# Performance work log

Measured on AMD Instinct MI355X. Metric: run time of the kernel, lower is better.

Reference implementation:

```python
import jax, jax.numpy as jnp
import numpy as np

N_NODES = 100000
N_EDGES = 640000
IN_CH = 128
HID = 128


def setup_inputs() -> dict:
    key = jax.random.key(0)
    k1, k2, k3, k4, k5 = jax.random.split(key, 5)
    z = jax.random.normal(k1, (N_NODES, IN_CH), dtype=jnp.float32)
    edge_index = jax.random.randint(k2, (2, N_EDGES), 0, N_NODES, dtype=jnp.int64)
    # Linear layers: stored as [in, out] for x @ W + b
    s1 = 1.0 / np.sqrt(2 * IN_CH)
    W1 = jax.random.uniform(k3, (2 * IN_CH, HID), minval=-s1, maxval=s1, dtype=jnp.float32)
    b1 = jnp.zeros((HID,), dtype=jnp.float32)
    s2 = 1.0 / np.sqrt(HID)
    W2 = jax.random.uniform(k4, (HID, 1), minval=-s2, maxval=s2, dtype=jnp.float32)
    b2 = jnp.zeros((1,), dtype=jnp.float32)
    return {"z": z, "edge_index": edge_index, "W1": W1, "b1": b1, "W2": W2, "b2": b2}


def reference(z, edge_index, W1, b1, W2, b2):
    # gather source/destination node embeddings and concat -> [E, 2*C]
    h = jnp.concatenate([z[edge_index[0]], z[edge_index[1]]], axis=-1)
    h = jax.nn.relu(h @ W1 + b1)  # [E, HID]; Dropout(0.2) is identity in eval
    out = h @ W2 + b2             # [E, 1]
    return out.squeeze(-1)        # [E]
```

## Files before the change

### kernel.cpp

```cpp
#include <hip/hip_runtime.h>
#include <hip/hip_bf16.h>

typedef short bf16x8 __attribute__((ext_vector_type(8)));
typedef float f32x4  __attribute__((ext_vector_type(4)));
typedef unsigned short u16;

static __device__ __forceinline__ u16 f2bf(float f) {
    unsigned u = __float_as_uint(f);
    u += 0x7FFFu + ((u >> 16) & 1u);
    return (u16)(u >> 16);
}
static __device__ __forceinline__ float bf2f(u16 b) {
    return __uint_as_float(((unsigned)b) << 16);
}
static __device__ __forceinline__ unsigned pack2(float lo, float hi) {
    return (unsigned)f2bf(lo) | ((unsigned)f2bf(hi) << 16);
}

#define BM 64
__global__ __launch_bounds__(256, 2) void node_gemm(
    const float* __restrict__ z,
    const float* __restrict__ W1,
    const float* __restrict__ b1,
    u16*         __restrict__ PQ,
    int M, int ntiles)
{
    __shared__ char As[BM * 256];
    __shared__ char Cb[BM * 512];
    const int tid  = threadIdx.x;
    const int lane = tid & 63;
    const int wave = tid >> 6;
    const int g    = lane >> 4;
    const int ln   = lane & 15;
    const int c0   = wave * 64;

    int t = blockIdx.x;
    if (t >= ntiles) return;

    bf16x8 af[4][4];
    #pragma unroll
    for (int ci = 0; ci < 4; ++ci) {
        int c = c0 + ci * 16 + ln;
        const float* src = (c < 128) ? (W1 + c) : (W1 + 128 * 128 + (c - 128));
        #pragma unroll
        for (int ks = 0; ks < 4; ++ks) {
            bf16x8 v;
            #pragma unroll
            for (int j = 0; j < 8; ++j)
                v[j] = (short)f2bf(src[(ks * 32 + g * 8 + j) * 128]);
            af[ks][ci] = v;
        }
    }

    float4 bias[4];
    #pragma unroll
    for (int ci = 0; ci < 4; ++ci) {
        int col = c0 + ci * 16 + g * 4;
        bias[ci] = (col < 128) ? *(const float4*)(b1 + col)
                               : make_float4(0.f, 0.f, 0.f, 0.f);
    }

    float4 r[8];

    {
        int m0 = t * BM;
        #pragma unroll
        for (int i = 0; i < 8; ++i) {
            int ci = tid + i * 256, row = ci >> 5, c4 = ci & 31;
            r[i] = make_float4(0.f, 0.f, 0.f, 0.f);
            if (m0 + row < M)
                r[i] = *(const float4*)(z + (size_t)(m0 + row) * 128 + c4 * 4);
        }
        #pragma unroll
        for (int i = 0; i < 8; ++i) {
            int ci = tid + i * 256, row = ci >> 5, c4 = ci & 31;
            ushort4 b;
            b.x = f2bf(r[i].x); b.y = f2bf(r[i].y);
            b.z = f2bf(r[i].z); b.w = f2bf(r[i].w);
            *(ushort4*)(As + row * 256 + ((c4 * 8) ^ ((row & 7) << 4))) = b;
        }
    }
    __syncthreads();

    while (true) {
        int next = t + gridDim.x;
        bool have = (next < ntiles);

        if (have) {
            int m0 = next * BM;
            #pragma unroll
            for (int i = 0; i < 8; ++i) {
                int ci = tid + i * 256, row = ci >> 5, c4 = ci & 31;
                r[i] = make_float4(0.f, 0.f, 0.f, 0.f);
                if (m0 + row < M)
                    r[i] = *(const float4*)(z + (size_t)(m0 + row) * 128 + c4 * 4);
            }
        }

        f32x4 acc[4][4];
        #pragma unroll
        for (int mf = 0; mf < 4; ++mf)
            #pragma unroll
            for (int ci = 0; ci < 4; ++ci)
                acc[mf][ci] = (f32x4){0.f, 0.f, 0.f, 0.f};
        #pragma unroll
        for (int ks = 0; ks < 4; ++ks) {
            #pragma unroll
            for (int mf = 0; mf < 4; ++mf) {
                int row  = mf * 16 + ln;
                int byte = row * 256 + ((ks * 64 + g * 16) ^ ((row & 7) << 4));
                bf16x8 b = *(const bf16x8*)(As + byte);
                #pragma unroll
                for (int ci = 0; ci < 4; ++ci)
                    acc[mf][ci] = __builtin_amdgcn_mfma_f32_16x16x32_bf16(
                        af[ks][ci], b, acc[mf][ci], 0, 0, 0);
            }
        }

        #pragma unroll
        for (int mf = 0; mf < 4; ++mf) {
            int node = mf * 16 + ln;
            #pragma unroll
            for (int ci = 0; ci < 4; ++ci) {
                int col = c0 + ci * 16 + g * 4;
                uint2 w;
                w.x = pack2(acc[mf][ci][0] + bias[ci].x,
                            acc[mf][ci][1] + bias[ci].y);
                w.y = pack2(acc[mf][ci][2] + bias[ci].z,
                            acc[mf][ci][3] + bias[ci].w);
                *(uint2*)(Cb + node * 512 + ((col * 2) ^ ((node & 7) << 4))) = w;
            }
        }
        __syncthreads();

        {
            int m0 = t * BM;
            int chunk = tid & 31;
            int nb    = tid >> 5;
            #pragma unroll
            for (int it = 0; it < 8; ++it) {
                int node = it * 8 + nb;
                uint4 v = *(const uint4*)(Cb + node * 512 +
                                          ((chunk * 16) ^ ((node & 7) << 4)));
                if (m0 + node < M)
                    *(uint4*)(PQ + (size_t)(m0 + node) * 256 + chunk * 8) = v;
            }
        }

        if (have) {
            #pragma unroll
            for (int i = 0; i < 8; ++i) {
                int ci = tid + i * 256, row = ci >> 5, c4 = ci & 31;
                ushort4 b;
                b.x = f2bf(r[i].x); b.y = f2bf(r[i].y);
                b.z = f2bf(r[i].z); b.w = f2bf(r[i].w);
                *(ushort4*)(As + row * 256 + ((c4 * 8) ^ ((row & 7) << 4))) = b;
            }
        } else {
            break;
        }
        __syncthreads();
        t = next;
    }
}

__global__ __launch_bounds__(256) void edge_mlp(
    const int* __restrict__ ei,
    const u16* __restrict__ PQ,
    const float* __restrict__ W2,
    const float* __restrict__ b2,
    float* __restrict__ out,
    int E)
{
    int gid = blockIdx.x * 256 + threadIdx.x;
    int e0  = (gid >> 4) * 4;
    int sub = gid & 15;
    if (e0 >= E) return;

    float4 w2a = *(const float4*)(W2 + sub * 8);
    float4 w2b = *(const float4*)(W2 + sub * 8 + 4);
    float ww[8] = {w2a.x, w2a.y, w2a.z, w2a.w, w2b.x, w2b.y, w2b.z, w2b.w};
    float bias = b2[0];

    if (e0 + 3 < E) {
        int4 s = *(const int4*)(ei + e0);
        int4 d = *(const int4*)(ei + E + e0);
        uint4 p0 = *(const uint4*)(PQ + (size_t)s.x * 256 + sub * 8);
        uint4 p1 = *(const uint4*)(PQ + (size_t)s.y * 256 + sub * 8);
        uint4 p2 = *(const uint4*)(PQ + (size_t)s.z * 256 + sub * 8);
        uint4 p3 = *(const uint4*)(PQ + (size_t)s.w * 256 + sub * 8);
        uint4 q0 = *(const uint4*)(PQ + (size_t)d.x * 256 + 128 + sub * 8);
        uint4 q1 = *(const uint4*)(PQ + (size_t)d.y * 256 + 128 + sub * 8);
        uint4 q2 = *(const uint4*)(PQ + (size_t)d.z * 256 + 128 + sub * 8);
        uint4 q3 = *(const uint4*)(PQ + (size_t)d.w * 256 + 128 + sub * 8);

        float a0 = 0.f, a1 = 0.f, a2 = 0.f, a3 = 0.f;
        const u16* pu0 = (const u16*)&p0; const u16* qu0 = (const u16*)&q0;
        const u16* pu1 = (const u16*)&p1; const u16* qu1 = (const u16*)&q1;
        const u16* pu2 = (const u16*)&p2; const u16* qu2 = (const u16*)&q2;
        const u16* pu3 = (const u16*)&p3; const u16* qu3 = (const u16*)&q3;
        #pragma unroll
        for (int j = 0; j < 8; ++j) {
            a0 = fmaf(fmaxf(bf2f(pu0[j]) + bf2f(qu0[j]), 0.f), ww[j], a0);
            a1 = fmaf(fmaxf(bf2f(pu1[j]) + bf2f(qu1[j]), 0.f), ww[j], a1);
            a2 = fmaf(fmaxf(bf2f(pu2[j]) + bf2f(qu2[j]), 0.f), ww[j], a2);
            a3 = fmaf(fmaxf(bf2f(pu3[j]) + bf2f(qu3[j]), 0.f), ww[j], a3);
        }
        #pragma unroll
        for (int m = 1; m < 16; m <<= 1) {
            a0 += __shfl_xor(a0, m);
            a1 += __shfl_xor(a1, m);
            a2 += __shfl_xor(a2, m);
            a3 += __shfl_xor(a3, m);
        }
        if (sub == 0) {
            float4 o = make_float4(a0 + bias, a1 + bias, a2 + bias, a3 + bias);
            *(float4*)(out + e0) = o;
        }
    } else {
        for (int k = 0; k < 4; ++k) {
            int e = e0 + k;
            if (e >= E) break;
            int sn = ei[e], dn = ei[E + e];
            uint4 p = *(const uint4*)(PQ + (size_t)sn * 256 + sub * 8);
            uint4 q = *(const uint4*)(PQ + (size_t)dn * 256 + 128 + sub * 8);
            const u16* pu = (const u16*)&p; const u16* qu = (const u16*)&q;
            float acc = 0.f;
            #pragma unroll
            for (int j = 0; j < 8; ++j)
                acc = fmaf(fmaxf(bf2f(pu[j]) + bf2f(qu[j]), 0.f), ww[j], acc);
            #pragma unroll
            for (int m = 1; m < 16; m <<= 1) acc += __shfl_xor(acc, m);
            if (sub == 0) out[e] = acc + bias;
        }
    }
}

extern "C" void kernel_launch(void* const* d_in, const int* in_sizes, int n_in,
                              void* d_out, int out_size, void* d_ws, size_t ws_size,
                              hipStream_t stream) {
    const float* z  = (const float*)d_in[0];
    const int*   ei = (const int*)d_in[1];
    const float* W1 = (const float*)d_in[2];
    const float* b1 = (const float*)d_in[3];
    const float* W2 = (const float*)d_in[4];
    const float* b2 = (const float*)d_in[5];
    float* out = (float*)d_out;

    const int M = in_sizes[0] / 128;
    const int E = in_sizes[1] / 2;

    u16* PQ = (u16*)d_ws;

    int ntiles = (M + BM - 1) / BM;
    int gb = ntiles < 512 ? ntiles : 512;
    hipLaunchKernelGGL(node_gemm, dim3(gb), dim3(256), 0, stream,
                       z, W1, b1, PQ, M, ntiles);

    int eb = ((E + 3) / 4 * 16 + 255) / 256;
    hipLaunchKernelGGL(edge_mlp, dim3(eb), dim3(256), 0, stream,
                       ei, PQ, W2, b2, out, E);
}
```

Baseline: 71.80 us.

## Partition edges by source-node range per block to localize gathers

Adds an edge kernel in which each of 8 block groups scans edge chunks, compacts via ballot and shared-memory queue the edges whose source node falls in its node range, then gathers P/Q rows and computes outputs. The goal is to improve cache locality of source-row gathers, possibly per XCD. It costs an 8x re-read of source indices, extra syncs and atomics, and scattered output writes. The fallback kernel is simplified to a scalar per-edge loop.

```diff
diff --git a/kernel.cpp b/kernel.cpp
--- a/kernel.cpp
+++ b/kernel.cpp
@@ -4,6 +4,7 @@
 typedef short bf16x8 __attribute__((ext_vector_type(8)));
 typedef float f32x4  __attribute__((ext_vector_type(4)));
 typedef unsigned short u16;
+typedef unsigned long long u64;
 
 static __device__ __forceinline__ u16 f2bf(float f) {
     unsigned u = __float_as_uint(f);
@@ -61,7 +62,6 @@
     }
 
     float4 r[8];
-
     {
         int m0 = t * BM;
         #pragma unroll
@@ -164,75 +164,153 @@
     }
 }
 
-__global__ __launch_bounds__(256) void edge_mlp(
+#define FCH 2048
+__global__ __launch_bounds__(256) void edge_mlp_filter(
     const int* __restrict__ ei,
     const u16* __restrict__ PQ,
     const float* __restrict__ W2,
     const float* __restrict__ b2,
     float* __restrict__ out,
-    int E)
+    int E, int M)
+{
+    __shared__ u64 q[512];
+    __shared__ int qn;
+    __shared__ int pn;
+
+    const int tid  = threadIdx.x;
+    const int myb  = blockIdx.x & 7;
+    const int chnk = blockIdx.x >> 3;
+    const int bsz  = (M + 7) >> 3;
+    const int lo   = myb * bsz;
+    const int hi   = (lo + bsz < M) ? (lo + bsz) : M;
+    const int sub  = tid & 15;
+    const int grp  = tid >> 4;
+
+    float4 w2a = *(const float4*)(W2 + sub * 8);
+    float4 w2b = *(const float4*)(W2 + sub * 8 + 4);
+    float ww[8] = {w2a.x, w2a.y, w2a.z, w2a.w, w2b.x, w2b.y, w2b.z, w2b.w};
+    float bias = b2[0];
+
+    if (tid == 0) qn = 0;
+    __syncthreads();
+
+    const int e0 = chnk * FCH;
+    #pragma unroll 1
+    for (int r = 0; r < FCH / 256; ++r) {
+        int e = e0 + r * 256 + tid;
+        int s = 0, d = 0;
+        bool mine = false;
+        if (e < E) {
+            s = ei[e];
+            if (s >= lo && s < hi) { mine = true; d = ei[E + e]; }
+        }
+        u64 mask = __ballot(mine);
+        int rank = __popcll(mask & ((1ULL << (tid & 63)) - 1ULL));
+        int wcnt = __popcll(mask);
+        int wb = 0;
+        if ((tid & 63) == 0 && wcnt) wb = atomicAdd(&qn, wcnt);
+        wb = __shfl(wb, 0);
+        if (mine)
+            q[wb + rank] = (u64)(unsigned)s | ((u64)(unsigned)d << 17)
+                         | ((u64)(unsigned)e << 34);
+        __syncthreads();
+
+        bool flush = (qn > 256) || (r == FCH / 256 - 1);
+        if (flush) {
+            if (tid == 0) { pn = qn; qn = 0; }
+            __syncthreads();
+            int n = pn;
+            for (int base = grp * 4; base < n; base += 64) {
+                if (base + 4 <= n) {
+                    u64 v0 = q[base], v1 = q[base + 1];
+                    u64 v2 = q[base + 2], v3 = q[base + 3];
+                    unsigned s0 = (unsigned)(v0 & 0x1FFFF), d0 = (unsigned)((v0 >> 17) & 0x1FFFF);
+                    unsigned s1 = (unsigned)(v1 & 0x1FFFF), d1 = (unsigned)((v1 >> 17) & 0x1FFFF);
+                    unsigned s2 = (unsigned)(v2 & 0x1FFFF), d2 = (unsigned)((v2 >> 17) & 0x1FFFF);
+                    unsigned s3 = (unsigned)(v3 & 0x1FFFF), d3 = (unsigned)((v3 >> 17) & 0x1FFFF);
+                    uint4 p0 = *(const uint4*)(PQ + (size_t)s0 * 256 + sub * 8);
+                    uint4 p1 = *(const uint4*)(PQ + (size_t)s1 * 256 + sub * 8);
+                    uint4 p2 = *(const uint4*)(PQ + (size_t)s2 * 256 + sub * 8);
+                    uint4 p3 = *(const uint4*)(PQ + (size_t)s3 * 256 + sub * 8);
+                    uint4 q0 = *(const uint4*)(PQ + (size_t)d0 * 256 + 128 + sub * 8);
+                    uint4 q1 = *(const uint4*)(PQ + (size_t)d1 * 256 + 128 + sub * 8);
+                    uint4 q2 = *(const uint4*)(PQ + (size_t)d2 * 256 + 128 + sub * 8);
+                    uint4 q3 = *(const uint4*)(PQ + (size_t)d3 * 256 + 128 + sub * 8);
+                    float a0 = 0.f, a1 = 0.f, a2 = 0.f, a3 = 0.f;
+                    const u16* pu0 = (const u16*)&p0; const u16* qu0 = (const u16*)&q0;
+                    const u16* pu1 = (const u16*)&p1; const u16* qu1 = (const u16*)&q1;
+                    const u16* pu2 = (const u16*)&p2; const u16* qu2 = (const u16*)&q2;
+                    const u16* pu3 = (const u16*)&p3; const u16* qu3 = (const u16*)&q3;
+                    #pragma unroll
+                    for (int j = 0; j < 8; ++j) {
+                        a0 = fmaf(fmaxf(bf2f(pu0[j]) + bf2f(qu0[j]), 0.f), ww[j], a0);
+                        a1 = fmaf(fmaxf(bf2f(pu1[j]) + bf2f(qu1[j]), 0.f), ww[j], a1);
+                        a2 = fmaf(fmaxf(bf2f(pu2[j]) + bf2f(qu2[j]), 0.f), ww[j], a2);
+                        a3 = fmaf(fmaxf(bf2f(pu3[j]) + bf2f(qu3[j]), 0.f), ww[j], a3);
+                    }
+                    #pragma unroll
+                    for (int m = 1; m < 16; m <<= 1) {
+                        a0 += __shfl_xor(a0, m);
+                        a1 += __shfl_xor(a1, m);
+                        a2 += __shfl_xor(a2, m);
+                        a3 += __shfl_xor(a3, m);
+                    }
+                    if (sub == 0) {
+                        out[(unsigned)(v0 >> 34)] = a0 + bias;
+                        out[(unsigned)(v1 >> 34)] = a1 + bias;
+                        out[(unsigned)(v2 >> 34)] = a2 + bias;
+                        out[(unsigned)(v3 >> 34)] = a3 + bias;
+                    }
+                } else {
+                    for (int i = base; i < n; ++i) {
+                        u64 v = q[i];
+                        unsigned s_ = (unsigned)(v & 0x1FFFF);
+                        unsigned d_ = (unsigned)((v >> 17) & 0x1FFFF);
+                        uint4 p = *(const uint4*)(PQ + (size_t)s_ * 256 + sub * 8);
+                        uint4 qq = *(const uint4*)(PQ + (size_t)d_ * 256 + 128 + sub * 8);
+                        const u16* pu = (const u16*)&p; const u16* qu = (const u16*)&qq;
+                        float acc = 0.f;
+                        #pragma unroll
+                        for (int j = 0; j < 8; ++j)
+                            acc = fmaf(fmaxf(bf2f(pu[j]) + bf2f(qu[j]), 0.f), ww[j], acc);
+                        #pragma unroll
+                        for (int m = 1; m < 16; m <<= 1) acc += __shfl_xor(acc, m);
+                        if (sub == 0) out[(unsigned)(v >> 34)] = acc + bias;
+                    }
+                }
+            }
+            __syncthreads();
+        }
+    }
+}
+
+__global__ __launch_bounds__(256) void edge_mlp(
+    const int* __restrict__ ei, const u16* __restrict__ PQ,
+    const float* __restrict__ W2, const float* __restrict__ b2,
+    float* __restrict__ out, int E)
 {
     int gid = blockIdx.x * 256 + threadIdx.x;
     int e0  = (gid >> 4) * 4;
     int sub = gid & 15;
     if (e0 >= E) return;
-
     float4 w2a = *(const float4*)(W2 + sub * 8);
     float4 w2b = *(const float4*)(W2 + sub * 8 + 4);
     float ww[8] = {w2a.x, w2a.y, w2a.z, w2a.w, w2b.x, w2b.y, w2b.z, w2b.w};
     float bias = b2[0];
-
-    if (e0 + 3 < E) {
-        int4 s = *(const int4*)(ei + e0);
-        int4 d = *(const int4*)(ei + E + e0);
-        uint4 p0 = *(const uint4*)(PQ + (size_t)s.x * 256 + sub * 8);
-        uint4 p1 = *(const uint4*)(PQ + (size_t)s.y * 256 + sub * 8);
-        uint4 p2 = *(const uint4*)(PQ + (size_t)s.z * 256 + sub * 8);
-        uint4 p3 = *(const uint4*)(PQ + (size_t)s.w * 256 + sub * 8);
-        uint4 q0 = *(const uint4*)(PQ + (size_t)d.x * 256 + 128 + sub * 8);
-        uint4 q1 = *(const uint4*)(PQ + (size_t)d.y * 256 + 128 + sub * 8);
-        uint4 q2 = *(const uint4*)(PQ + (size_t)d.z * 256 + 128 + sub * 8);
-        uint4 q3 = *(const uint4*)(PQ + (size_t)d.w * 256 + 128 + sub * 8);
-
-        float a0 = 0.f, a1 = 0.f, a2 = 0.f, a3 = 0.f;
-        const u16* pu0 = (const u16*)&p0; const u16* qu0 = (const u16*)&q0;
-        const u16* pu1 = (const u16*)&p1; const u16* qu1 = (const u16*)&q1;
-        const u16* pu2 = (const u16*)&p2; const u16* qu2 = (const u16*)&q2;
-        const u16* pu3 = (const u16*)&p3; const u16* qu3 = (const u16*)&q3;
-        #pragma unroll
-        for (int j = 0; j < 8; ++j) {
-            a0 = fmaf(fmaxf(bf2f(pu0[j]) + bf2f(qu0[j]), 0.f), ww[j], a0);
-            a1 = fmaf(fmaxf(bf2f(pu1[j]) + bf2f(qu1[j]), 0.f), ww[j], a1);
-            a2 = fmaf(fmaxf(bf2f(pu2[j]) + bf2f(qu2[j]), 0.f), ww[j], a2);
-            a3 = fmaf(fmaxf(bf2f(pu3[j]) + bf2f(qu3[j]), 0.f), ww[j], a3);
-        }
-        #pragma unroll
-        for (int m = 1; m < 16; m <<= 1) {
-            a0 += __shfl_xor(a0, m);
-            a1 += __shfl_xor(a1, m);
-            a2 += __shfl_xor(a2, m);
-            a3 += __shfl_xor(a3, m);
-        }
-        if (sub == 0) {
-            float4 o = make_float4(a0 + bias, a1 + bias, a2 + bias, a3 + bias);
-            *(float4*)(out + e0) = o;
-        }
-    } else {
-        for (int k = 0; k < 4; ++k) {
-            int e = e0 + k;
-            if (e >= E) break;
-            int sn = ei[e], dn = ei[E + e];
-            uint4 p = *(const uint4*)(PQ + (size_t)sn * 256 + sub * 8);
-            uint4 q = *(const uint4*)(PQ + (size_t)dn * 256 + 128 + sub * 8);
-            const u16* pu = (const u16*)&p; const u16* qu = (const u16*)&q;
-            float acc = 0.f;
-            #pragma unroll
-            for (int j = 0; j < 8; ++j)
-                acc = fmaf(fmaxf(bf2f(pu[j]) + bf2f(qu[j]), 0.f), ww[j], acc);
-            #pragma unroll
-            for (int m = 1; m < 16; m <<= 1) acc += __shfl_xor(acc, m);
-            if (sub == 0) out[e] = acc + bias;
-        }
+    for (int k = 0; k < 4; ++k) {
+        int e = e0 + k;
+        if (e >= E) break;
+        int sn = ei[e], dn = ei[E + e];
+        uint4 p = *(const uint4*)(PQ + (size_t)sn * 256 + sub * 8);
+        uint4 q = *(const uint4*)(PQ + (size_t)dn * 256 + 128 + sub * 8);
+        const u16* pu = (const u16*)&p; const u16* qu = (const u16*)&q;
+        float acc = 0.f;
+        #pragma unroll
+        for (int j = 0; j < 8; ++j)
+            acc = fmaf(fmaxf(bf2f(pu[j]) + bf2f(qu[j]), 0.f), ww[j], acc);
+        #pragma unroll
+        for (int m = 1; m < 16; m <<= 1) acc += __shfl_xor(acc, m);
+        if (sub == 0) out[e] = acc + bias;
     }
 }
 
@@ -257,7 +335,13 @@
     hipLaunchKernelGGL(node_gemm, dim3(gb), dim3(256), 0, stream,
                        z, W1, b1, PQ, M, ntiles);
 
-    int eb = ((E + 3) / 4 * 16 + 255) / 256;
-    hipLaunchKernelGGL(edge_mlp, dim3(eb), dim3(256), 0, stream,
-                       ei, PQ, W2, b2, out, E);
-}
+    if (M < (1 << 17) && E < (1 << 20)) {
+        int nch = (E + FCH - 1) / FCH;
+        hipLaunchKernelGGL(edge_mlp_filter, dim3(nch * 8), dim3(256), 0, stream,
+                           ei, PQ, W2, b2, out, E, M);
+    } else {
+        int eb = ((E + 3) / 4 * 16 + 255) / 256;
+        hipLaunchKernelGGL(edge_mlp, dim3(eb), dim3(256), 0, stream,
+                           ei, PQ, W2, b2, out, E);
+    }
+}
```

After: 76.96 us. +7.2%, slower.
